# Performance work log

Hardware: AMD Instinct MI355X
Metric: run time of the kernel (lower is better)

The kernel has to match this reference:

```python
import jax, jax.numpy as jnp
import numpy as np

N = 100000
E = 2000000
LN_EPS = 1e-5


def _ln(x, g, b):
    m = jnp.mean(x, axis=-1, keepdims=True)
    v = jnp.mean((x - m) ** 2, axis=-1, keepdims=True)
    return (x - m) * jax.lax.rsqrt(v + LN_EPS) * g + b


def _gcn_conv(x, W, b, row, col, n_nodes):
    xw = x @ W  # [N, out_dim]
    deg = jax.ops.segment_sum(jnp.ones((row.shape[0],), xw.dtype), row, num_segments=n_nodes) + 1.0
    dinv = jax.lax.rsqrt(deg)
    norm = dinv[row] * dinv[col]  # [E]
    msg = xw[col] * norm[:, None]  # gather + scale, [E, out_dim]
    agg = jax.ops.segment_sum(msg, row, num_segments=n_nodes)
    self_loop = xw * (dinv * dinv)[:, None]
    return agg + self_loop + b


def setup_inputs() -> dict:
    key = jax.random.key(0)
    ks = jax.random.split(key, 32)
    s = 0.05
    d = dict(
        coords=jax.random.normal(ks[0], (N, 2), jnp.float32),
        features=jax.random.normal(ks[1], (N, 3), jnp.float32),
        edge_index=jax.random.randint(ks[2], (2, E), 0, N, jnp.int32),
        # spatial encoder FFN: 2->128, two hidden 128->128 (relu+LN), last 128->128 (relu)
        fw0=jax.random.normal(ks[3], (2, 128), jnp.float32) * s,
        fb0=jnp.zeros((128,), jnp.float32),
        fg0=jnp.ones((128,), jnp.float32),
        fe0=jnp.zeros((128,), jnp.float32),
        fw1=jax.random.normal(ks[4], (128, 128), jnp.float32) * s,
        fb1=jnp.zeros((128,), jnp.float32),
        fg1=jnp.ones((128,), jnp.float32),
        fe1=jnp.zeros((128,), jnp.float32),
        fw2=jax.random.normal(ks[5], (128, 128), jnp.float32) * s,
        fb2=jnp.zeros((128,), jnp.float32),
        fg2=jnp.ones((128,), jnp.float32),
        fe2=jnp.zeros((128,), jnp.float32),
        fw3=jax.random.normal(ks[6], (128, 128), jnp.float32) * s,
        fb3=jnp.zeros((128,), jnp.float32),
        # dec: 128->64->32->16 with tanh between
        dw0=jax.random.normal(ks[7], (128, 64), jnp.float32) * s,
        db0=jnp.zeros((64,), jnp.float32),
        dw1=jax.random.normal(ks[8], (64, 32), jnp.float32) * s,
        db1=jnp.zeros((32,), jnp.float32),
        dw2=jax.random.normal(ks[9], (32, 16), jnp.float32) * s,
        db2=jnp.zeros((16,), jnp.float32),
        # GCN convs: (3+16)->64, 64->64; fc 64->1
        cw1=jax.random.normal(ks[10], (19, 64), jnp.float32) * s,
        cb1=jnp.zeros((64,), jnp.float32),
        cw2=jax.random.normal(ks[11], (64, 64), jnp.float32) * s,
        cb2=jnp.zeros((64,), jnp.float32),
        ow=jax.random.normal(ks[12], (64, 1), jnp.float32) * s,
        ob=jnp.zeros((1,), jnp.float32),
    )
    return d


def reference(coords, features, edge_index,
              fw0, fb0, fg0, fe0, fw1, fb1, fg1, fe1, fw2, fb2, fg2, fe2, fw3, fb3,
              dw0, db0, dw1, db1, dw2, db2,
              cw1, cb1, cw2, cb2, ow, ob):
    # positional encoder FFN (dropout disabled / eval mode)
    h = _ln(jax.nn.relu(coords @ fw0 + fb0), fg0, fe0)
    h = _ln(jax.nn.relu(h @ fw1 + fb1), fg1, fe1)
    h = _ln(jax.nn.relu(h @ fw2 + fb2), fg2, fe2)
    h = jax.nn.relu(h @ fw3 + fb3)
    # decoder to emb_dim
    emb = jnp.tanh(h @ dw0 + db0)
    emb = jnp.tanh(emb @ dw1 + db1)
    emb = emb @ dw2 + db2  # [N, 16]
    x = jnp.concatenate([features, emb], axis=-1)  # [N, 19]
    row, col = edge_index[0], edge_index[1]
    h1 = jax.nn.relu(_gcn_conv(x, cw1, cb1, row, col, x.shape[0]))
    h2 = _gcn_conv(h1, cw2, cb2, row, col, x.shape[0])
    out = h2 @ ow + ob  # [N, 1]
    return out
```

## Files before the change

kernel.cpp:

```cpp
#include <hip/hip_runtime.h>
#include <hip/hip_bf16.h>
#include <math.h>

#define TM 64
#define XROW 64
#define NSEG 8

typedef float v2f __attribute__((ext_vector_type(2)));
typedef float f32x4 __attribute__((ext_vector_type(4)));
typedef __bf16 bf16x8 __attribute__((ext_vector_type(8)));
typedef unsigned short u16x8 __attribute__((ext_vector_type(8)));
typedef unsigned int uint_t;
typedef unsigned short ushort_t;

__device__ __forceinline__ v2f fma2(v2f a, v2f b, v2f c) {
    return __builtin_elementwise_fma(a, b, c);
}
__device__ __forceinline__ v2f splat2(float s) { return (v2f){s, s}; }
__device__ __forceinline__ v2f max02(v2f a) {
    return (v2f){fmaxf(a.x, 0.0f), fmaxf(a.y, 0.0f)};
}
__device__ __forceinline__ uint_t pack_bf16(float lo, float hi) {
    uint_t r;
    asm volatile("v_cvt_pk_bf16_f32 %0, %1, %2" : "=v"(r) : "v"(lo), "v"(hi));
    return r;
}
__device__ __forceinline__ float bf16_f(ushort_t u) {
    union { uint_t i; float f; } c; c.i = ((uint_t)u) << 16; return c.f;
}
__device__ __forceinline__ float blo(uint_t u) {
    union { uint_t i; float f; } c; c.i = u << 16; return c.f;
}
__device__ __forceinline__ float bhi(uint_t u) {
    union { uint_t i; float f; } c; c.i = u & 0xffff0000u; return c.f;
}

__device__ __forceinline__ int aaddr(int node, int feat) {
    return (node * 256 + feat * 2) ^ ((node & 15) << 4);
}

__global__ void deg8_prep_kernel(const int* __restrict__ row, int* __restrict__ cnt8,
                                 int E_, int Nn, int NE,
                                 const float* __restrict__ W1, const float* __restrict__ W2,
                                 const float* __restrict__ W3, ushort_t* __restrict__ outw,
                                 const float* __restrict__ cw2, const float* __restrict__ cb2,
                                 const float* __restrict__ ow, const float* __restrict__ ob,
                                 float* __restrict__ wb) {
    int bid = blockIdx.x;
    if (bid < NE) {
        int s = bid & (NSEG - 1);
        int* cs = cnt8 + (size_t)s * Nn;
        int e4 = (bid * 256 + threadIdx.x) * 4;
        if (e4 + 3 < E_) {
            int4 r = *(const int4*)&row[e4];
            atomicAdd(&cs[r.x], 1); atomicAdd(&cs[r.y], 1);
            atomicAdd(&cs[r.z], 1); atomicAdd(&cs[r.w], 1);
        } else {
            for (int e = e4; e < E_; e++) atomicAdd(&cs[row[e]], 1);
        }
        return;
    }
    int pid = bid - NE;
    if (pid == 384) {
        int i = threadIdx.x;
        if (i < 64) {
            float a = 0.f;
            for (int j = 0; j < 64; j++) a += cw2[i * 64 + j] * ow[j];
            wb[i] = a;
        }
        if (i == 0) {
            float bb = 0.f;
            for (int j = 0; j < 64; j++) bb += cb2[j] * ow[j];
            wb[64] = bb + ob[0];
        }
        return;
    }
    int gid = pid * 256 + threadIdx.x;
    int layer = gid >> 15;
    int idx   = gid & 32767;
    const float* W = (layer == 0) ? W1 : (layer == 1) ? W2 : W3;
    int j    = idx & 7;
    int lane = (idx >> 3) & 63;
    int rest = idx >> 9;
    int cb   = rest & 7;
    int r2   = rest >> 3;
    int kk   = r2 & 3;
    int h    = r2 >> 2;
    int k = kk * 32 + (lane >> 4) * 8 + j;
    int n = cb * 16 + (lane & 15);
    float wv = W[k * 128 + n];
    ushort_t hi = (ushort_t)pack_bf16(wv, wv);
    ushort_t v;
    if (h == 0) v = hi;
    else {
        float res = wv - bf16_f(hi);
        v = (ushort_t)pack_bf16(res, res);
    }
    outw[(size_t)layer * 32768 + idx] = v;
}

__global__ __launch_bounds__(256, 4) void scatter_ffn_kernel(
    const int* __restrict__ row, const int* __restrict__ col,
    int* __restrict__ fill8, int* __restrict__ es, int E_, int NE,
    const float* __restrict__ coords, const float* __restrict__ features,
    const float* __restrict__ dinv,
    const float* __restrict__ fw0, const float* __restrict__ fb0,
    const float* __restrict__ fg0, const float* __restrict__ fe0,
    const ushort_t* __restrict__ wswz,
    const float* __restrict__ fb1, const float* __restrict__ fg1, const float* __restrict__ fe1,
    const float* __restrict__ fb2, const float* __restrict__ fg2, const float* __restrict__ fe2,
    const float* __restrict__ fb3,
    const float* __restrict__ dw0, const float* __restrict__ db0,
    const float* __restrict__ dw1, const float* __restrict__ db1,
    const float* __restrict__ dw2, const float* __restrict__ db2,
    char* __restrict__ xsb, int n_nodes)
{
    __shared__ __align__(16) char abuf[16384];
    __shared__ __align__(16) ushort_t tbuf[128][64];

    const int bid = blockIdx.x;
    const int t   = threadIdx.x;

    if (bid < NE) {
        int s = bid & (NSEG - 1);
        int Nn = n_nodes;
        int* fs = fill8 + (size_t)s * Nn;
        int e4 = (bid * 256 + t) * 4;
        if (e4 + 3 < E_) {
            int4 r = *(const int4*)&row[e4];
            int4 c = *(const int4*)&col[e4];
            es[atomicAdd(&fs[r.x], 1)] = c.x;
            es[atomicAdd(&fs[r.y], 1)] = c.y;
            es[atomicAdd(&fs[r.z], 1)] = c.z;
            es[atomicAdd(&fs[r.w], 1)] = c.w;
        } else {
            for (int e = e4; e < E_; e++) {
                int p = atomicAdd(&fs[row[e]], 1);
                es[p] = col[e];
            }
        }
        return;
    }

    const int lane = t & 63;
    const int w    = __builtin_amdgcn_readfirstlane(t >> 6);
    const int jw   = w * 32;
    const int n0   = (bid - NE) * TM;

    int g = n0 + lane;
    if (g >= n_nodes) g = n_nodes - 1;

    {
        float* ps1 = (float*)tbuf;
        float* ps2 = ((float*)tbuf) + 256;
        v2f acc[16];
        float2 c = *(const float2*)&coords[(size_t)g * 2];
        v2f cx = splat2(c.x), cy = splat2(c.y);
        #pragma unroll
        for (int q = 0; q < 16; q++) {
            int j = jw + 2 * q;
            v2f w0 = *(const v2f*)&fw0[j];
            v2f w1 = *(const v2f*)&fw0[128 + j];
            v2f bb = *(const v2f*)&fb0[j];
            acc[q] = max02(fma2(cx, w0, fma2(cy, w1, bb)));
        }
        float s1 = 0.f, s2 = 0.f;
        #pragma unroll
        for (int q = 0; q < 16; q++) {
            s1 += acc[q].x + acc[q].y;
            s2 += acc[q].x * acc[q].x + acc[q].y * acc[q].y;
        }
        ps1[w * 64 + lane] = s1; ps2[w * 64 + lane] = s2;
        __syncthreads();
        float t1 = ps1[lane] + ps1[64 + lane] + ps1[128 + lane] + ps1[192 + lane];
        float t2 = ps2[lane] + ps2[64 + lane] + ps2[128 + lane] + ps2[192 + lane];
        float mean = t1 * (1.0f / 128.0f);
        float var  = t2 * (1.0f / 128.0f) - mean * mean;
        float inv  = rsqrtf(var + 1e-5f);
        v2f mean2 = splat2(mean), inv2 = splat2(inv);
        #pragma unroll
        for (int q = 0; q < 16; q++) {
            int j = jw + 2 * q;
            v2f gm = *(const v2f*)&fg0[j];
            v2f bt = *(const v2f*)&fe0[j];
            v2f o = fma2((acc[q] - mean2) * inv2, gm, bt);
            *(uint_t*)(abuf + aaddr(lane, j)) = pack_bf16(o.x, o.y);
        }
        __syncthreads();
    }

    auto mfma_layer = [&](const ushort_t* Wb, const float* __restrict__ bias) {
        f32x4 acc[2][4] = {};
        #pragma unroll
        for (int kk = 0; kk < 4; kk++) {
            bf16x8 B[2][2];
            #pragma unroll
            for (int cb2 = 0; cb2 < 2; cb2++) {
                int cb = 2 * w + cb2;
                #pragma unroll
                for (int h = 0; h < 2; h++) {
                    const ushort_t* p = Wb + (size_t)(((h * 4 + kk) * 8 + cb) * 64 + lane) * 8;
                    B[cb2][h] = *(const bf16x8*)p;
                }
            }
            #pragma unroll
            for (int rb = 0; rb < 4; rb++) {
                int node = rb * 16 + (lane & 15);
                bf16x8 A = *(const bf16x8*)(abuf + aaddr(node, kk * 32 + (lane >> 4) * 8));
                #pragma unroll
                for (int cb2 = 0; cb2 < 2; cb2++) {
                    acc[cb2][rb] = __builtin_amdgcn_mfma_f32_16x16x32_bf16(A, B[cb2][0], acc[cb2][rb], 0, 0, 0);
                    acc[cb2][rb] = __builtin_amdgcn_mfma_f32_16x16x32_bf16(A, B[cb2][1], acc[cb2][rb], 0, 0, 0);
                }
            }
        }
        __syncthreads();
        float bv0 = bias[jw + (lane & 15)];
        float bv1 = bias[jw + 16 + (lane & 15)];
        #pragma unroll
        for (int cb2 = 0; cb2 < 2; cb2++) {
            int col2 = jw + cb2 * 16 + (lane & 15);
            float bv = cb2 ? bv1 : bv0;
            #pragma unroll
            for (int rb = 0; rb < 4; rb++) {
                #pragma unroll
                for (int r = 0; r < 4; r++) {
                    float v = fmaxf(acc[cb2][rb][r] + bv, 0.0f);
                    int node = rb * 16 + (lane >> 4) * 4 + r;
                    *(ushort_t*)(abuf + aaddr(node, col2)) = (ushort_t)pack_bf16(v, v);
                }
            }
        }
        __syncthreads();
    };

    auto ln_pass = [&](const float* __restrict__ gam, const float* __restrict__ bet) {
        int node = t >> 2;
        int part = t & 3;
        float vals[32];
        float s1 = 0.f, s2 = 0.f;
        #pragma unroll
        for (int q = 0; q < 4; q++) {
            int f0 = part * 32 + q * 8;
            u16x8 u = *(const u16x8*)(abuf + aaddr(node, f0));
            #pragma unroll
            for (int i = 0; i < 8; i++) {
                float v = bf16_f(u[i]);
                vals[q * 8 + i] = v;
                s1 += v; s2 += v * v;
            }
        }
        s1 += __shfl_xor(s1, 1); s1 += __shfl_xor(s1, 2);
        s2 += __shfl_xor(s2, 1); s2 += __shfl_xor(s2, 2);
        float mean = s1 * (1.0f / 128.0f);
        float var  = s2 * (1.0f / 128.0f) - mean * mean;
        float inv  = rsqrtf(var + 1e-5f);
        #pragma unroll
        for (int q = 0; q < 4; q++) {
            int f0 = part * 32 + q * 8;
            uint_t ov[4];
            #pragma unroll
            for (int p = 0; p < 4; p++) {
                v2f gm = *(const v2f*)&gam[f0 + 2 * p];
                v2f bt = *(const v2f*)&bet[f0 + 2 * p];
                float a = (vals[q * 8 + 2 * p]     - mean) * inv * gm.x + bt.x;
                float b = (vals[q * 8 + 2 * p + 1] - mean) * inv * gm.y + bt.y;
                ov[p] = pack_bf16(a, b);
            }
            uint4 uv = make_uint4(ov[0], ov[1], ov[2], ov[3]);
            *(uint4*)(abuf + aaddr(node, f0)) = uv;
        }
        __syncthreads();
    };

    mfma_layer(wswz,         fb1); ln_pass(fg1, fe1);
    mfma_layer(wswz + 32768, fb2); ln_pass(fg2, fe2);
    mfma_layer(wswz + 65536, fb3);

    {
        #pragma unroll
        for (int q = 0; q < 4; q++) {
            int f0 = jw + q * 8;
            u16x8 u = *(const u16x8*)(abuf + aaddr(lane, f0));
            #pragma unroll
            for (int i = 0; i < 8; i++) tbuf[f0 + i][lane] = u[i];
        }
        __syncthreads();
    }

    {
        const float2* src = (const float2*)dw0;
        uint_t* dst = (uint_t*)abuf;
        #pragma unroll
        for (int q = 0; q < 16; q++) {
            int i = q * 256 + t;
            float2 v = src[i];
            dst[i] = pack_bf16(v.x, v.y);
        }
        __syncthreads();
    }

    {
        const int j16 = w * 16;
        v2f d0[8];
        #pragma unroll
        for (int q = 0; q < 8; q++) d0[q] = *(const v2f*)&db0[j16 + 2 * q];
        const uint4* wd = (const uint4*)abuf;
        #pragma unroll 4
        for (int k = 0; k < 128; k++) {
            v2f av = splat2(bf16_f(tbuf[k][lane]));
            uint4 u0 = wd[k * 8 + w * 2];
            uint4 u1 = wd[k * 8 + w * 2 + 1];
            d0[0] = fma2(av, (v2f){blo(u0.x), bhi(u0.x)}, d0[0]);
            d0[1] = fma2(av, (v2f){blo(u0.y), bhi(u0.y)}, d0[1]);
            d0[2] = fma2(av, (v2f){blo(u0.z), bhi(u0.z)}, d0[2]);
            d0[3] = fma2(av, (v2f){blo(u0.w), bhi(u0.w)}, d0[3]);
            d0[4] = fma2(av, (v2f){blo(u1.x), bhi(u1.x)}, d0[4]);
            d0[5] = fma2(av, (v2f){blo(u1.y), bhi(u1.y)}, d0[5]);
            d0[6] = fma2(av, (v2f){blo(u1.z), bhi(u1.z)}, d0[6]);
            d0[7] = fma2(av, (v2f){blo(u1.w), bhi(u1.w)}, d0[7]);
        }
        #pragma unroll
        for (int q = 0; q < 8; q++) d0[q] = (v2f){tanhf(d0[q].x), tanhf(d0[q].y)};
        __syncthreads();
        #pragma unroll
        for (int q = 0; q < 8; q++) {
            uint_t r = pack_bf16(d0[q].x, d0[q].y);
            tbuf[j16 + 2 * q][lane]     = (ushort_t)r;
            tbuf[j16 + 2 * q + 1][lane] = (ushort_t)(r >> 16);
        }
        __syncthreads();
    }

    {
        const int j8 = w * 8;
        v2f d1[4];
        #pragma unroll
        for (int q = 0; q < 4; q++) d1[q] = *(const v2f*)&db1[j8 + 2 * q];
        #pragma unroll 4
        for (int k = 0; k < 64; k++) {
            v2f av = splat2(bf16_f(tbuf[k][lane]));
            const v2f* W2 = (const v2f*)(dw1 + k * 32 + j8);
            #pragma unroll
            for (int q = 0; q < 4; q++) d1[q] = fma2(av, W2[q], d1[q]);
        }
        #pragma unroll
        for (int q = 0; q < 4; q++) d1[q] = (v2f){tanhf(d1[q].x), tanhf(d1[q].y)};
        __syncthreads();
        #pragma unroll
        for (int q = 0; q < 4; q++) {
            uint_t r = pack_bf16(d1[q].x, d1[q].y);
            tbuf[j8 + 2 * q][lane]     = (ushort_t)r;
            tbuf[j8 + 2 * q + 1][lane] = (ushort_t)(r >> 16);
        }
        __syncthreads();
    }

    {
        const int j4 = w * 4;
        v2f d2[2];
        #pragma unroll
        for (int q = 0; q < 2; q++) d2[q] = *(const v2f*)&db2[j4 + 2 * q];
        #pragma unroll 4
        for (int k = 0; k < 32; k++) {
            v2f av = splat2(bf16_f(tbuf[k][lane]));
            const v2f* W2 = (const v2f*)(dw2 + k * 16 + j4);
            d2[0] = fma2(av, W2[0], d2[0]);
            d2[1] = fma2(av, W2[1], d2[1]);
        }
        __syncthreads();
        #pragma unroll
        for (int q = 0; q < 2; q++) {
            uint_t r = pack_bf16(d2[q].x, d2[q].y);
            tbuf[j4 + 2 * q][lane]     = (ushort_t)r;
            tbuf[j4 + 2 * q + 1][lane] = (ushort_t)(r >> 16);
        }
        __syncthreads();
    }

    {
        const int nn = t & 63;
        const int jg = t >> 6;
        int gg = n0 + nn;
        if (gg < n_nodes && jg < 3) {
            float dgg = dinv[gg];
            char* rp = xsb + (size_t)gg * XROW;
            if (jg == 0) {
                float4 f;
                f.x = features[(size_t)gg * 3 + 0] * dgg;
                f.y = features[(size_t)gg * 3 + 1] * dgg;
                f.z = features[(size_t)gg * 3 + 2] * dgg;
                f.w = 0.0f;
                *(float4*)rp = f;
            } else {
                int e0 = (jg - 1) * 8;
                uint_t u[4];
                #pragma unroll
                for (int p = 0; p < 4; p++) {
                    float lo = bf16_f(tbuf[e0 + 2 * p][nn]) * dgg;
                    float hi = bf16_f(tbuf[e0 + 2 * p + 1][nn]) * dgg;
                    u[p] = pack_bf16(lo, hi);
                }
                uint4 uv = make_uint4(u[0], u[1], u[2], u[3]);
                *(uint4*)(rp + 16 + (jg - 1) * 16) = uv;
            }
        }
    }
}

__global__ void scan1_kernel(const int* __restrict__ in, int* __restrict__ out,
                             int* __restrict__ bsum, int n) {
    __shared__ int tmp[256];
    int t = threadIdx.x, b = blockIdx.x;
    int base = b * 2048 + t * 8;
    int v[8]; int s = 0;
    #pragma unroll
    for (int q = 0; q < 8; q++) {
        int idx = base + q;
        v[q] = (idx < n) ? in[idx] : 0;
        s += v[q];
    }
    tmp[t] = s; __syncthreads();
    #pragma unroll
    for (int d = 1; d < 256; d <<= 1) {
        int add = (t >= d) ? tmp[t - d] : 0;
        __syncthreads();
        tmp[t] += add;
        __syncthreads();
    }
    int run = tmp[t] - s;
    #pragma unroll
    for (int q = 0; q < 8; q++) {
        int idx = base + q;
        if (idx < n) out[idx] = run;
        run += v[q];
    }
    if (t == 255) bsum[b] = tmp[t];
}

__global__ void scan2_kernel(int* __restrict__ bsum, int B) {
    __shared__ int tmp[512];
    int t = threadIdx.x;
    tmp[t] = (t < B) ? bsum[t] : 0; __syncthreads();
    #pragma unroll
    for (int d = 1; d < 512; d <<= 1) {
        int add = (t >= d) ? tmp[t - d] : 0;
        __syncthreads();
        tmp[t] += add;
        __syncthreads();
    }
    if (t < B) bsum[t] = tmp[t];
}

__global__ void scanfix_dinv_kernel(int* __restrict__ data, const int* __restrict__ bsum,
                                    const int* __restrict__ cnt8, float* __restrict__ dinv,
                                    int n, int Nn) {
    int i = blockIdx.x * 256 + threadIdx.x;
    if (i < n) {
        int b = i >> 11;
        if (b > 0) data[i] += bsum[b - 1];
    }
    if (i < Nn) {
        int s = 0;
        #pragma unroll
        for (int q = 0; q < NSEG; q++) s += cnt8[(size_t)q * Nn + i];
        dinv[i] = rsqrtf((float)s + 1.0f);
    }
}

__global__ __launch_bounds__(256) void node1g_kernel(
    const int* __restrict__ fill8, const int* __restrict__ cnt8, const int* __restrict__ es,
    const float* __restrict__ dinv, const char* __restrict__ xsb,
    const float* __restrict__ cw1, const float* __restrict__ cb1,
    const float* __restrict__ wb, float* __restrict__ ss, int n)
{
    __shared__ float w[19 * 64];
    __shared__ float bbs[64];
    __shared__ float wes[64];
    for (int i = threadIdx.x; i < 19 * 64; i += 256) w[i] = cw1[i];
    for (int i = threadIdx.x; i < 64; i += 256) { bbs[i] = cb1[i]; wes[i] = wb[i]; }
    __syncthreads();
    const int t  = threadIdx.x;
    const int oc = t & 7;
    const int i  = blockIdx.x * 32 + (t >> 3);
    if (i >= n) return;
    const float di = dinv[i];

    float af[19];
    #pragma unroll
    for (int q = 0; q < 19; q++) af[q] = 0.f;

    auto addrow = [&](const char* rp) {
        float4 F = *(const float4*)rp;
        uint4 U0 = *(const uint4*)(rp + 16);
        uint4 U1 = *(const uint4*)(rp + 32);
        af[0] += F.x; af[1] += F.y; af[2] += F.z;
        af[3]  += blo(U0.x); af[4]  += bhi(U0.x);
        af[5]  += blo(U0.y); af[6]  += bhi(U0.y);
        af[7]  += blo(U0.z); af[8]  += bhi(U0.z);
        af[9]  += blo(U0.w); af[10] += bhi(U0.w);
        af[11] += blo(U1.x); af[12] += bhi(U1.x);
        af[13] += blo(U1.y); af[14] += bhi(U1.y);
        af[15] += blo(U1.z); af[16] += bhi(U1.z);
        af[17] += blo(U1.w); af[18] += bhi(U1.w);
    };

    if (oc == 0) addrow(xsb + (size_t)i * XROW);
    const int end = fill8[(size_t)oc * n + i];
    const int dgs = cnt8[(size_t)oc * n + i];
    for (int e = end - dgs; e < end; e++) {
        int c = es[e];
        addrow(xsb + (size_t)c * XROW);
    }

    float a19[19];
    #pragma unroll
    for (int q = 0; q < 19; q++) {
        float v = af[q];
        v += __shfl_xor(v, 1);
        v += __shfl_xor(v, 2);
        v += __shfl_xor(v, 4);
        a19[q] = v * di;
    }

    const int j0 = oc * 8;
    v2f am[4];
    const v2f* w2  = (const v2f*)w;
    const v2f* bb2 = (const v2f*)bbs;
    #pragma unroll
    for (int q = 0; q < 4; q++) am[q] = bb2[j0 / 2 + q];
    #pragma unroll
    for (int k = 0; k < 19; k++) {
        v2f v = splat2(a19[k]);
        #pragma unroll
        for (int q = 0; q < 4; q++) am[q] = fma2(v, w2[k * 32 + j0 / 2 + q], am[q]);
    }
    const v2f* we2 = (const v2f*)wes;
    v2f sv2 = {0.f, 0.f};
    #pragma unroll
    for (int q = 0; q < 4; q++) sv2 = fma2(max02(am[q]), we2[j0 / 2 + q], sv2);
    float sv = sv2.x + sv2.y;
    sv += __shfl_xor(sv, 1);
    sv += __shfl_xor(sv, 2);
    sv += __shfl_xor(sv, 4);
    if (oc == 0) ss[i] = di * sv;
}

__global__ __launch_bounds__(256) void outg_kernel(
    const int* __restrict__ fill8, const int* __restrict__ cnt8, const int* __restrict__ es,
    const float* __restrict__ dinv, const float* __restrict__ ss,
    const float* __restrict__ wb, float* __restrict__ out, int n)
{
    const int t  = threadIdx.x;
    const int oc = t & 7;
    const int i  = blockIdx.x * 32 + (t >> 3);
    if (i >= n) return;
    const int end = fill8[(size_t)oc * n + i];
    const int dgs = cnt8[(size_t)oc * n + i];
    float sum = (oc == 0) ? ss[i] : 0.f;
    for (int e = end - dgs; e < end; e++) {
        int c = es[e];
        sum += ss[c];
    }
    sum += __shfl_xor(sum, 1);
    sum += __shfl_xor(sum, 2);
    sum += __shfl_xor(sum, 4);
    if (oc == 0) out[i] = wb[64] + dinv[i] * sum;
}

extern "C" void kernel_launch(void* const* d_in, const int* in_sizes, int n_in,
                              void* d_out, int out_size, void* d_ws, size_t ws_size,
                              hipStream_t stream) {
    const float* coords   = (const float*)d_in[0];
    const float* features = (const float*)d_in[1];
    const int*   eidx     = (const int*)d_in[2];
    const float* fw0 = (const float*)d_in[3];
    const float* fb0 = (const float*)d_in[4];
    const float* fg0 = (const float*)d_in[5];
    const float* fe0 = (const float*)d_in[6];
    const float* fw1 = (const float*)d_in[7];
    const float* fb1 = (const float*)d_in[8];
    const float* fg1 = (const float*)d_in[9];
    const float* fe1 = (const float*)d_in[10];
    const float* fw2 = (const float*)d_in[11];
    const float* fb2 = (const float*)d_in[12];
    const float* fg2 = (const float*)d_in[13];
    const float* fe2 = (const float*)d_in[14];
    const float* fw3 = (const float*)d_in[15];
    const float* fb3 = (const float*)d_in[16];
    const float* dw0 = (const float*)d_in[17];
    const float* db0 = (const float*)d_in[18];
    const float* dw1 = (const float*)d_in[19];
    const float* db1 = (const float*)d_in[20];
    const float* dw2 = (const float*)d_in[21];
    const float* db2 = (const float*)d_in[22];
    const float* cw1 = (const float*)d_in[23];
    const float* cb1 = (const float*)d_in[24];
    const float* cw2 = (const float*)d_in[25];
    const float* cb2 = (const float*)d_in[26];
    const float* ow  = (const float*)d_in[27];
    const float* ob  = (const float*)d_in[28];
    float* out = (float*)d_out;

    const int Nn = in_sizes[0] / 2;
    const int E_ = in_sizes[2] / 2;
    const int n8 = NSEG * Nn;
    const int NBS = (n8 + 2047) / 2048;
    const int NO = (Nn * 8 + 255) / 256;
    const int NT = (Nn + TM - 1) / TM;
    const int NE = (E_ / 4 + 255) / 256;

    char* ws = (char*)d_ws;
    size_t o = 0;
    char*  xsb   = (char*) (ws + o); o += (size_t)Nn * XROW;
    int*   cnt8  = (int*)  (ws + o); o += (size_t)n8 * sizeof(int);
    int*   fill8 = (int*)  (ws + o); o += (size_t)n8 * sizeof(int);
    int*   bsum  = (int*)  (ws + o); o += 512 * sizeof(int);
    float* dinv  = (float*)(ws + o); o += (size_t)Nn * sizeof(float);
    float* ssb   = (float*)(ws + o); o += (size_t)Nn * sizeof(float);
    int*   es    = (int*)  (ws + o); o += (size_t)E_ * sizeof(int);
    float* wb    = (float*)(ws + o); o += 80 * sizeof(float);
    o = (o + 15) & ~(size_t)15;
    ushort_t* wswz = (ushort_t*)(ws + o); o += 3 * 32768 * sizeof(ushort_t);

    hipMemsetAsync(cnt8, 0, (size_t)n8 * sizeof(int), stream);

    deg8_prep_kernel<<<NE + 385, 256, 0, stream>>>(eidx, cnt8, E_, Nn, NE,
                                                   fw1, fw2, fw3, wswz,
                                                   cw2, cb2, ow, ob, wb);
    scan1_kernel<<<NBS, 256, 0, stream>>>(cnt8, fill8, bsum, n8);
    scan2_kernel<<<1, 512, 0, stream>>>(bsum, NBS);
    scanfix_dinv_kernel<<<(n8 + 255) / 256, 256, 0, stream>>>(fill8, bsum, cnt8, dinv, n8, Nn);

    scatter_ffn_kernel<<<NE + NT, 256, 0, stream>>>(
        eidx, eidx + E_, fill8, es, E_, NE,
        coords, features, dinv,
        fw0, fb0, fg0, fe0,
        wswz,
        fb1, fg1, fe1, fb2, fg2, fe2, fb3,
        dw0, db0, dw1, db1, dw2, db2, xsb, Nn);

    node1g_kernel<<<NO, 256, 0, stream>>>(fill8, cnt8, es, dinv, xsb, cw1, cb1, wb, ssb, Nn);
    outg_kernel<<<NO, 256, 0, stream>>>(fill8, cnt8, es, dinv, ssb, wb, out, Nn);
}
```

Baseline: 375.0 us.

## Fuse weight prep, degree count and FFN into cooperative persistent kernel

Replaces the memset, degree/prep kernel and FFN part of the scatter kernel with one cooperative persistent kernel. It zeroes counters and swizzles weights, then after a grid sync runs degree counting on 128 blocks while the other blocks compute the FFN tiles. The dinv scaling of xsb moves into a new kernel that also performs the edge scatter, so the FFN no longer has to wait for the scan. The scan is retuned to 4096 elements per block. The cost is an extra read-modify-write pass over xsb, a grid sync, and a fixed split between degree and FFN blocks that may balance poorly.

Result: slower. 685.5 us (+82.8%).

```diff
diff --git a/kernel.cpp b/kernel.cpp
--- a/kernel.cpp
+++ b/kernel.cpp
@@ -1,10 +1,14 @@
 #include <hip/hip_runtime.h>
 #include <hip/hip_bf16.h>
+#include <hip/hip_cooperative_groups.h>
 #include <math.h>
+
+namespace cg = cooperative_groups;
 
 #define TM 64
 #define XROW 64
 #define NSEG 8
+#define DEGB 128
 
 typedef float v2f __attribute__((ext_vector_type(2)));
 typedef float f32x4 __attribute__((ext_vector_type(4)));
@@ -34,134 +38,47 @@
 __device__ __forceinline__ float bhi(uint_t u) {
     union { uint_t i; float f; } c; c.i = u & 0xffff0000u; return c.f;
 }
-
 __device__ __forceinline__ int aaddr(int node, int feat) {
     return (node * 256 + feat * 2) ^ ((node & 15) << 4);
 }
 
-__global__ void deg8_prep_kernel(const int* __restrict__ row, int* __restrict__ cnt8,
-                                 int E_, int Nn, int NE,
-                                 const float* __restrict__ W1, const float* __restrict__ W2,
-                                 const float* __restrict__ W3, ushort_t* __restrict__ outw,
-                                 const float* __restrict__ cw2, const float* __restrict__ cb2,
-                                 const float* __restrict__ ow, const float* __restrict__ ob,
-                                 float* __restrict__ wb) {
-    int bid = blockIdx.x;
-    if (bid < NE) {
-        int s = bid & (NSEG - 1);
-        int* cs = cnt8 + (size_t)s * Nn;
-        int e4 = (bid * 256 + threadIdx.x) * 4;
-        if (e4 + 3 < E_) {
-            int4 r = *(const int4*)&row[e4];
-            atomicAdd(&cs[r.x], 1); atomicAdd(&cs[r.y], 1);
-            atomicAdd(&cs[r.z], 1); atomicAdd(&cs[r.w], 1);
-        } else {
-            for (int e = e4; e < E_; e++) atomicAdd(&cs[row[e]], 1);
-        }
-        return;
-    }
-    int pid = bid - NE;
-    if (pid == 384) {
-        int i = threadIdx.x;
-        if (i < 64) {
-            float a = 0.f;
-            for (int j = 0; j < 64; j++) a += cw2[i * 64 + j] * ow[j];
-            wb[i] = a;
-        }
-        if (i == 0) {
-            float bb = 0.f;
-            for (int j = 0; j < 64; j++) bb += cb2[j] * ow[j];
-            wb[64] = bb + ob[0];
-        }
-        return;
-    }
-    int gid = pid * 256 + threadIdx.x;
-    int layer = gid >> 15;
-    int idx   = gid & 32767;
-    const float* W = (layer == 0) ? W1 : (layer == 1) ? W2 : W3;
-    int j    = idx & 7;
-    int lane = (idx >> 3) & 63;
-    int rest = idx >> 9;
-    int cb   = rest & 7;
-    int r2   = rest >> 3;
-    int kk   = r2 & 3;
-    int h    = r2 >> 2;
-    int k = kk * 32 + (lane >> 4) * 8 + j;
-    int n = cb * 16 + (lane & 15);
-    float wv = W[k * 128 + n];
-    ushort_t hi = (ushort_t)pack_bf16(wv, wv);
-    ushort_t v;
-    if (h == 0) v = hi;
-    else {
-        float res = wv - bf16_f(hi);
-        v = (ushort_t)pack_bf16(res, res);
-    }
-    outw[(size_t)layer * 32768 + idx] = v;
-}
-
-__global__ __launch_bounds__(256, 4) void scatter_ffn_kernel(
-    const int* __restrict__ row, const int* __restrict__ col,
-    int* __restrict__ fill8, int* __restrict__ es, int E_, int NE,
-    const float* __restrict__ coords, const float* __restrict__ features,
-    const float* __restrict__ dinv,
-    const float* __restrict__ fw0, const float* __restrict__ fb0,
-    const float* __restrict__ fg0, const float* __restrict__ fe0,
-    const ushort_t* __restrict__ wswz,
-    const float* __restrict__ fb1, const float* __restrict__ fg1, const float* __restrict__ fe1,
-    const float* __restrict__ fb2, const float* __restrict__ fg2, const float* __restrict__ fe2,
-    const float* __restrict__ fb3,
-    const float* __restrict__ dw0, const float* __restrict__ db0,
-    const float* __restrict__ dw1, const float* __restrict__ db1,
-    const float* __restrict__ dw2, const float* __restrict__ db2,
-    char* __restrict__ xsb, int n_nodes)
-{
-    __shared__ __align__(16) char abuf[16384];
-    __shared__ __align__(16) ushort_t tbuf[128][64];
-
-    const int bid = blockIdx.x;
-    const int t   = threadIdx.x;
-
-    if (bid < NE) {
-        int s = bid & (NSEG - 1);
-        int Nn = n_nodes;
-        int* fs = fill8 + (size_t)s * Nn;
-        int e4 = (bid * 256 + t) * 4;
-        if (e4 + 3 < E_) {
-            int4 r = *(const int4*)&row[e4];
-            int4 c = *(const int4*)&col[e4];
-            es[atomicAdd(&fs[r.x], 1)] = c.x;
-            es[atomicAdd(&fs[r.y], 1)] = c.y;
-            es[atomicAdd(&fs[r.z], 1)] = c.z;
-            es[atomicAdd(&fs[r.w], 1)] = c.w;
-        } else {
-            for (int e = e4; e < E_; e++) {
-                int p = atomicAdd(&fs[row[e]], 1);
-                es[p] = col[e];
-            }
-        }
-        return;
-    }
-
+struct MA {
+    const int* row; const int* col;
+    const float* coords; const float* features;
+    const float* fw0; const float* fb0; const float* fg0; const float* fe0;
+    const float* fw1; const float* fw2; const float* fw3;
+    const float* fb1; const float* fg1; const float* fe1;
+    const float* fb2; const float* fg2; const float* fe2;
+    const float* fb3;
+    const float* dw0; const float* db0;
+    const float* dw1; const float* db1;
+    const float* dw2; const float* db2;
+    const float* cw2; const float* cb2; const float* ow; const float* ob;
+    int* cnt8; float* wb; ushort_t* wswz; char* xsb;
+    int E; int Nn; int NCH; int NT; int n8;
+};
+
+__device__ void ffn_tile(const MA& a, int tile, int t, char* abuf, ushort_t (*tbuf)[64]) {
     const int lane = t & 63;
     const int w    = __builtin_amdgcn_readfirstlane(t >> 6);
     const int jw   = w * 32;
-    const int n0   = (bid - NE) * TM;
+    const int n0   = tile * TM;
 
     int g = n0 + lane;
-    if (g >= n_nodes) g = n_nodes - 1;
+    if (g >= a.Nn) g = a.Nn - 1;
 
     {
         float* ps1 = (float*)tbuf;
         float* ps2 = ((float*)tbuf) + 256;
         v2f acc[16];
-        float2 c = *(const float2*)&coords[(size_t)g * 2];
+        float2 c = *(const float2*)&a.coords[(size_t)g * 2];
         v2f cx = splat2(c.x), cy = splat2(c.y);
         #pragma unroll
         for (int q = 0; q < 16; q++) {
             int j = jw + 2 * q;
-            v2f w0 = *(const v2f*)&fw0[j];
-            v2f w1 = *(const v2f*)&fw0[128 + j];
-            v2f bb = *(const v2f*)&fb0[j];
+            v2f w0 = *(const v2f*)&a.fw0[j];
+            v2f w1 = *(const v2f*)&a.fw0[128 + j];
+            v2f bb = *(const v2f*)&a.fb0[j];
             acc[q] = max02(fma2(cx, w0, fma2(cy, w1, bb)));
         }
         float s1 = 0.f, s2 = 0.f;
@@ -181,8 +98,8 @@
         #pragma unroll
         for (int q = 0; q < 16; q++) {
             int j = jw + 2 * q;
-            v2f gm = *(const v2f*)&fg0[j];
-            v2f bt = *(const v2f*)&fe0[j];
+            v2f gm = *(const v2f*)&a.fg0[j];
+            v2f bt = *(const v2f*)&a.fe0[j];
             v2f o = fma2((acc[q] - mean2) * inv2, gm, bt);
             *(uint_t*)(abuf + aaddr(lane, j)) = pack_bf16(o.x, o.y);
         }
@@ -263,9 +180,9 @@
             for (int p = 0; p < 4; p++) {
                 v2f gm = *(const v2f*)&gam[f0 + 2 * p];
                 v2f bt = *(const v2f*)&bet[f0 + 2 * p];
-                float a = (vals[q * 8 + 2 * p]     - mean) * inv * gm.x + bt.x;
-                float b = (vals[q * 8 + 2 * p + 1] - mean) * inv * gm.y + bt.y;
-                ov[p] = pack_bf16(a, b);
+                float x = (vals[q * 8 + 2 * p]     - mean) * inv * gm.x + bt.x;
+                float y = (vals[q * 8 + 2 * p + 1] - mean) * inv * gm.y + bt.y;
+                ov[p] = pack_bf16(x, y);
             }
             uint4 uv = make_uint4(ov[0], ov[1], ov[2], ov[3]);
             *(uint4*)(abuf + aaddr(node, f0)) = uv;
@@ -273,9 +190,9 @@
         __syncthreads();
     };
 
-    mfma_layer(wswz,         fb1); ln_pass(fg1, fe1);
-    mfma_layer(wswz + 32768, fb2); ln_pass(fg2, fe2);
-    mfma_layer(wswz + 65536, fb3);
+    mfma_layer(a.wswz,         a.fb1); ln_pass(a.fg1, a.fe1);
+    mfma_layer(a.wswz + 32768, a.fb2); ln_pass(a.fg2, a.fe2);
+    mfma_layer(a.wswz + 65536, a.fb3);
 
     {
         #pragma unroll
@@ -289,7 +206,7 @@
     }
 
     {
-        const float2* src = (const float2*)dw0;
+        const float2* src = (const float2*)a.dw0;
         uint_t* dst = (uint_t*)abuf;
         #pragma unroll
         for (int q = 0; q < 16; q++) {
@@ -304,7 +221,7 @@
         const int j16 = w * 16;
         v2f d0[8];
         #pragma unroll
-        for (int q = 0; q < 8; q++) d0[q] = *(const v2f*)&db0[j16 + 2 * q];
+        for (int q = 0; q < 8; q++) d0[q] = *(const v2f*)&a.db0[j16 + 2 * q];
         const uint4* wd = (const uint4*)abuf;
         #pragma unroll 4
         for (int k = 0; k < 128; k++) {
@@ -336,11 +253,11 @@
         const int j8 = w * 8;
         v2f d1[4];
         #pragma unroll
-        for (int q = 0; q < 4; q++) d1[q] = *(const v2f*)&db1[j8 + 2 * q];
+        for (int q = 0; q < 4; q++) d1[q] = *(const v2f*)&a.db1[j8 + 2 * q];
         #pragma unroll 4
         for (int k = 0; k < 64; k++) {
             v2f av = splat2(bf16_f(tbuf[k][lane]));
-            const v2f* W2 = (const v2f*)(dw1 + k * 32 + j8);
+            const v2f* W2 = (const v2f*)(a.dw1 + k * 32 + j8);
             #pragma unroll
             for (int q = 0; q < 4; q++) d1[q] = fma2(av, W2[q], d1[q]);
         }
@@ -360,11 +277,11 @@
         const int j4 = w * 4;
         v2f d2[2];
         #pragma unroll
-        for (int q = 0; q < 2; q++) d2[q] = *(const v2f*)&db2[j4 + 2 * q];
+        for (int q = 0; q < 2; q++) d2[q] = *(const v2f*)&a.db2[j4 + 2 * q];
         #pragma unroll 4
         for (int k = 0; k < 32; k++) {
             v2f av = splat2(bf16_f(tbuf[k][lane]));
-            const v2f* W2 = (const v2f*)(dw2 + k * 16 + j4);
+            const v2f* W2 = (const v2f*)(a.dw2 + k * 16 + j4);
             d2[0] = fma2(av, W2[0], d2[0]);
             d2[1] = fma2(av, W2[1], d2[1]);
         }
@@ -382,28 +299,89 @@
         const int nn = t & 63;
         const int jg = t >> 6;
         int gg = n0 + nn;
-        if (gg < n_nodes && jg < 3) {
-            float dgg = dinv[gg];
-            char* rp = xsb + (size_t)gg * XROW;
+        if (gg < a.Nn && jg < 3) {
+            char* rp = a.xsb + (size_t)gg * XROW;
             if (jg == 0) {
                 float4 f;
-                f.x = features[(size_t)gg * 3 + 0] * dgg;
-                f.y = features[(size_t)gg * 3 + 1] * dgg;
-                f.z = features[(size_t)gg * 3 + 2] * dgg;
+                f.x = a.features[(size_t)gg * 3 + 0];
+                f.y = a.features[(size_t)gg * 3 + 1];
+                f.z = a.features[(size_t)gg * 3 + 2];
                 f.w = 0.0f;
                 *(float4*)rp = f;
             } else {
                 int e0 = (jg - 1) * 8;
                 uint_t u[4];
                 #pragma unroll
-                for (int p = 0; p < 4; p++) {
-                    float lo = bf16_f(tbuf[e0 + 2 * p][nn]) * dgg;
-                    float hi = bf16_f(tbuf[e0 + 2 * p + 1][nn]) * dgg;
-                    u[p] = pack_bf16(lo, hi);
-                }
-                uint4 uv = make_uint4(u[0], u[1], u[2], u[3]);
-                *(uint4*)(rp + 16 + (jg - 1) * 16) = uv;
-            }
+                for (int p = 0; p < 4; p++)
+                    u[p] = (uint_t)tbuf[e0 + 2 * p][nn] | ((uint_t)tbuf[e0 + 2 * p + 1][nn] << 16);
+                *(uint4*)(rp + 16 + (jg - 1) * 16) = make_uint4(u[0], u[1], u[2], u[3]);
+            }
+        }
+    }
+}
+
+__global__ __launch_bounds__(256, 4) void mega_kernel(MA a) {
+    __shared__ __align__(16) char smem[32768];
+    cg::grid_group grid = cg::this_grid();
+    const int t   = threadIdx.x;
+    const int bid = blockIdx.x;
+    const int G   = gridDim.x;
+
+    for (int i = bid * 256 + t; i < a.n8; i += G * 256) a.cnt8[i] = 0;
+    for (int gid = bid * 256 + t; gid < 3 * 32768; gid += G * 256) {
+        int layer = gid >> 15;
+        int idx   = gid & 32767;
+        const float* W = (layer == 0) ? a.fw1 : (layer == 1) ? a.fw2 : a.fw3;
+        int j    = idx & 7;
+        int lane = (idx >> 3) & 63;
+        int rest = idx >> 9;
+        int cb   = rest & 7;
+        int r2   = rest >> 3;
+        int kk   = r2 & 3;
+        int h    = r2 >> 2;
+        int k = kk * 32 + (lane >> 4) * 8 + j;
+        int n = cb * 16 + (lane & 15);
+        float wv = W[k * 128 + n];
+        ushort_t hi = (ushort_t)pack_bf16(wv, wv);
+        ushort_t v;
+        if (h == 0) v = hi;
+        else { float res = wv - bf16_f(hi); v = (ushort_t)pack_bf16(res, res); }
+        a.wswz[(size_t)layer * 32768 + idx] = v;
+    }
+    if (bid == 0) {
+        int i = t;
+        if (i < 64) {
+            float s = 0.f;
+            for (int j = 0; j < 64; j++) s += a.cw2[i * 64 + j] * a.ow[j];
+            a.wb[i] = s;
+        }
+        if (i == 0) {
+            float bb = 0.f;
+            for (int j = 0; j < 64; j++) bb += a.cb2[j] * a.ow[j];
+            a.wb[64] = bb + a.ob[0];
+        }
+    }
+    __threadfence();
+    grid.sync();
+
+    if (bid < DEGB) {
+        for (int c = bid; c < a.NCH; c += DEGB) {
+            int s = c & (NSEG - 1);
+            int* cs = a.cnt8 + (size_t)s * a.Nn;
+            int e4 = (c * 256 + t) * 4;
+            if (e4 + 3 < a.E) {
+                int4 r = *(const int4*)&a.row[e4];
+                atomicAdd(&cs[r.x], 1); atomicAdd(&cs[r.y], 1);
+                atomicAdd(&cs[r.z], 1); atomicAdd(&cs[r.w], 1);
+            } else {
+                for (int e = e4; e < a.E; e++) atomicAdd(&cs[a.row[e]], 1);
+            }
+        }
+    } else {
+        const int F = G - DEGB;
+        for (int tile = bid - DEGB; tile < a.NT; tile += F) {
+            __syncthreads();
+            ffn_tile(a, tile, t, smem, (ushort_t(*)[64])(smem + 16384));
         }
     }
 }
@@ -412,10 +390,10 @@
                              int* __restrict__ bsum, int n) {
     __shared__ int tmp[256];
     int t = threadIdx.x, b = blockIdx.x;
-    int base = b * 2048 + t * 8;
-    int v[8]; int s = 0;
-    #pragma unroll
-    for (int q = 0; q < 8; q++) {
+    int base = b * 4096 + t * 16;
+    int v[16]; int s = 0;
+    #pragma unroll
+    for (int q = 0; q < 16; q++) {
         int idx = base + q;
         v[q] = (idx < n) ? in[idx] : 0;
         s += v[q];
@@ -430,7 +408,7 @@
     }
     int run = tmp[t] - s;
     #pragma unroll
-    for (int q = 0; q < 8; q++) {
+    for (int q = 0; q < 16; q++) {
         int idx = base + q;
         if (idx < n) out[idx] = run;
         run += v[q];
@@ -439,11 +417,11 @@
 }
 
 __global__ void scan2_kernel(int* __restrict__ bsum, int B) {
-    __shared__ int tmp[512];
+    __shared__ int tmp[256];
     int t = threadIdx.x;
     tmp[t] = (t < B) ? bsum[t] : 0; __syncthreads();
     #pragma unroll
-    for (int d = 1; d < 512; d <<= 1) {
+    for (int d = 1; d < 256; d <<= 1) {
         int add = (t >= d) ? tmp[t - d] : 0;
         __syncthreads();
         tmp[t] += add;
@@ -457,7 +435,7 @@
                                     int n, int Nn) {
     int i = blockIdx.x * 256 + threadIdx.x;
     if (i < n) {
-        int b = i >> 11;
+        int b = i >> 12;
         if (b > 0) data[i] += bsum[b - 1];
     }
     if (i < Nn) {
@@ -466,6 +444,52 @@
         for (int q = 0; q < NSEG; q++) s += cnt8[(size_t)q * Nn + i];
         dinv[i] = rsqrtf((float)s + 1.0f);
     }
+}
+
+__global__ void scatxscale_kernel(const int* __restrict__ row, const int* __restrict__ col,
+                                  int* __restrict__ fill8, int* __restrict__ es,
+                                  const float* __restrict__ dinv, char* __restrict__ xsb,
+                                  int E_, int Nn, int NCH) {
+    int bid = blockIdx.x;
+    int t = threadIdx.x;
+    if (bid < NCH) {
+        int s = bid & (NSEG - 1);
+        int* fs = fill8 + (size_t)s * Nn;
+        int e4 = (bid * 256 + t) * 4;
+        if (e4 + 3 < E_) {
+            int4 r = *(const int4*)&row[e4];
+            int4 c = *(const int4*)&col[e4];
+            es[atomicAdd(&fs[r.x], 1)] = c.x;
+            es[atomicAdd(&fs[r.y], 1)] = c.y;
+            es[atomicAdd(&fs[r.z], 1)] = c.z;
+            es[atomicAdd(&fs[r.w], 1)] = c.w;
+        } else {
+            for (int e = e4; e < E_; e++) {
+                int p = atomicAdd(&fs[row[e]], 1);
+                es[p] = col[e];
+            }
+        }
+        return;
+    }
+    int r = (bid - NCH) * 256 + t;
+    if (r >= Nn) return;
+    float d = dinv[r];
+    char* rp = xsb + (size_t)r * XROW;
+    float4 F = *(float4*)rp;
+    F.x *= d; F.y *= d; F.z *= d;
+    *(float4*)rp = F;
+    uint4 U = *(uint4*)(rp + 16);
+    U.x = pack_bf16(blo(U.x) * d, bhi(U.x) * d);
+    U.y = pack_bf16(blo(U.y) * d, bhi(U.y) * d);
+    U.z = pack_bf16(blo(U.z) * d, bhi(U.z) * d);
+    U.w = pack_bf16(blo(U.w) * d, bhi(U.w) * d);
+    *(uint4*)(rp + 16) = U;
+    uint4 V = *(uint4*)(rp + 32);
+    V.x = pack_bf16(blo(V.x) * d, bhi(V.x) * d);
+    V.y = pack_bf16(blo(V.y) * d, bhi(V.y) * d);
+    V.z = pack_bf16(blo(V.z) * d, bhi(V.z) * d);
+    V.w = pack_bf16(blo(V.w) * d, bhi(V.w) * d);
+    *(uint4*)(rp + 32) = V;
 }
 
 __global__ __launch_bounds__(256) void node1g_kernel(
@@ -602,13 +626,14 @@
     const float* ob  = (const float*)d_in[28];
     float* out = (float*)d_out;
 
-    const int Nn = in_sizes[0] / 2;
-    const int E_ = in_sizes[2] / 2;
-    const int n8 = NSEG * Nn;
-    const int NBS = (n8 + 2047) / 2048;
-    const int NO = (Nn * 8 + 255) / 256;
-    const int NT = (Nn + TM - 1) / TM;
-    const int NE = (E_ / 4 + 255) / 256;
+    const int Nn  = in_sizes[0] / 2;
+    const int E_  = in_sizes[2] / 2;
+    const int n8  = NSEG * Nn;
+    const int NCH = (E_ / 4 + 255) / 256;
+    const int NT  = (Nn + TM - 1) / TM;
+    const int NSC = (n8 + 4095) / 4096;
+    const int NO  = (Nn * 8 + 255) / 256;
+    const int NSCL = (Nn + 255) / 256;
 
     char* ws = (char*)d_ws;
     size_t o = 0;
@@ -623,23 +648,36 @@
     o = (o + 15) & ~(size_t)15;
     ushort_t* wswz = (ushort_t*)(ws + o); o += 3 * 32768 * sizeof(ushort_t);
 
-    hipMemsetAsync(cnt8, 0, (size_t)n8 * sizeof(int), stream);
-
-    deg8_prep_kernel<<<NE + 385, 256, 0, stream>>>(eidx, cnt8, E_, Nn, NE,
-                                                   fw1, fw2, fw3, wswz,
-                                                   cw2, cb2, ow, ob, wb);
-    scan1_kernel<<<NBS, 256, 0, stream>>>(cnt8, fill8, bsum, n8);
-    scan2_kernel<<<1, 512, 0, stream>>>(bsum, NBS);
+    int nb = 0;
+    hipOccupancyMaxActiveBlocksPerMultiprocessor(&nb, mega_kernel, 256, 0);
+    if (nb < 1) nb = 1;
+    if (nb > 4) nb = 4;
+    int G = nb * 256;
+    G &= ~7;
+    if (G < DEGB + 8) G = DEGB + 8;
+
+    MA ma;
+    ma.row = eidx; ma.col = eidx + E_;
+    ma.coords = coords; ma.features = features;
+    ma.fw0 = fw0; ma.fb0 = fb0; ma.fg0 = fg0; ma.fe0 = fe0;
+    ma.fw1 = fw1; ma.fw2 = fw2; ma.fw3 = fw3;
+    ma.fb1 = fb1; ma.fg1 = fg1; ma.fe1 = fe1;
+    ma.fb2 = fb2; ma.fg2 = fg2; ma.fe2 = fe2;
+    ma.fb3 = fb3;
+    ma.dw0 = dw0; ma.db0 = db0;
+    ma.dw1 = dw1; ma.db1 = db1;
+    ma.dw2 = dw2; ma.db2 = db2;
+    ma.cw2 = cw2; ma.cb2 = cb2; ma.ow = ow; ma.ob = ob;
+    ma.cnt8 = cnt8; ma.wb = wb; ma.wswz = wswz; ma.xsb = xsb;
+    ma.E = E_; ma.Nn = Nn; ma.NCH = NCH; ma.NT = NT; ma.n8 = n8;
+
+    void* kargs[] = { (void*)&ma };
+    hipLaunchCooperativeKernel((void*)mega_kernel, dim3(G), dim3(256), kargs, 0, stream);
+
+    scan1_kernel<<<NSC, 256, 0, stream>>>(cnt8, fill8, bsum, n8);
+    scan2_kernel<<<1, 256, 0, stream>>>(bsum, NSC);
     scanfix_dinv_kernel<<<(n8 + 255) / 256, 256, 0, stream>>>(fill8, bsum, cnt8, dinv, n8, Nn);
-
-    scatter_ffn_kernel<<<NE + NT, 256, 0, stream>>>(
-        eidx, eidx + E_, fill8, es, E_, NE,
-        coords, features, dinv,
-        fw0, fb0, fg0, fe0,
-        wswz,
-        fb1, fg1, fe1, fb2, fg2, fe2, fb3,
-        dw0, db0, dw1, db1, dw2, db2, xsb, Nn);
-
+    scatxscale_kernel<<<NCH + NSCL, 256, 0, stream>>>(eidx, eidx + E_, fill8, es, dinv, xsb, E_, Nn, NCH);
     node1g_kernel<<<NO, 256, 0, stream>>>(fill8, cnt8, es, dinv, xsb, cw1, cb1, wb, ssb, Nn);
     outg_kernel<<<NO, 256, 0, stream>>>(fill8, cnt8, es, dinv, ssb, wb, out, Nn);
 }
```
